# Performance work log

Hardware: AMD Instinct MI355X
Metric: run time of the kernel (lower is better)

The kernel has to match this reference:

```python
import jax, jax.numpy as jnp
import numpy as np

# Module constants (from init_kwargs)
TRUNC = (32, 32, 32)
OUT_SIZE = (32, 32, 32)
HOMOMORPHIC = False


def dct2_ortho_mat(N):
    """Orthonormal DCT-II matrix C of shape [N, N]; y = C @ x along an axis.
    IDCT (DCT-III ortho) is C.T since C is orthogonal."""
    n = jnp.arange(N, dtype=jnp.float32)          # sample index
    k = n[:, None]                                 # frequency index
    C = jnp.cos(jnp.pi * (2.0 * n + 1.0) * k / (2.0 * N))
    scale = jnp.where(k == 0, jnp.sqrt(1.0 / N), jnp.sqrt(2.0 / N))
    return (C * scale).astype(jnp.float32)


def _transform3d(x, Cd, Ch, Cw):
    # Apply separable 1D transforms along D, H, W axes of [B, C, D, H, W].
    x = jnp.einsum('kd,bcdhw->bckhw', Cd, x)
    x = jnp.einsum('kh,bcdhw->bcdkw', Ch, x)
    x = jnp.einsum('kw,bcdhw->bcdhk', Cw, x)
    return x


def setup_inputs() -> dict:
    key = jax.random.key(0)
    x = jax.random.normal(key, (4, 32, 64, 64, 64), dtype=jnp.float32)
    return {"x": x}


def reference(x) -> jnp.ndarray:
    B, C, D, H, W = x.shape
    if HOMOMORPHIC:
        x = jnp.log(x + 1e-6)

    # 3D DCT-II (ortho) along D, H, W
    Cd, Ch, Cw = dct2_ortho_mat(D), dct2_ortho_mat(H), dct2_ortho_mat(W)
    x_dct = _transform3d(x, Cd, Ch, Cw)

    # Crop low frequencies to `truncation`, zero-pad up to `output_size`
    t0, t1, t2 = TRUNC
    o0, o1, o2 = OUT_SIZE
    x_crop = x_dct[:, :, :t0, :t1, :t2]
    x_pad = jnp.pad(x_crop, ((0, 0), (0, 0), (0, o0 - t0), (0, o1 - t1), (0, o2 - t2)))

    # 3D IDCT (DCT-III ortho) = transpose of the ortho DCT-II matrix
    Id, Ih, Iw = dct2_ortho_mat(o0).T, dct2_ortho_mat(o1).T, dct2_ortho_mat(o2).T
    out = _transform3d(x_pad, Id, Ih, Iw)

    if HOMOMORPHIC:
        out = jnp.exp(out)
    return out
```

## Files before the change

kernel.cpp:

```cpp
#include <hip/hip_runtime.h>
#include <math.h>
#include <stdint.h>


#define PI_F 3.14159265358979323846f

typedef __attribute__((ext_vector_type(4))) float f32x4;
typedef __attribute__((ext_vector_type(8))) short bf16x8;

union U16x8 { uint4 q; bf16x8 v; };

__device__ __forceinline__ unsigned short bf16r(float x) {
    union { float f; uint32_t u; } c; c.f = x;
    uint32_t r = (c.u + 0x7FFFu + ((c.u >> 16) & 1u)) >> 16;
    return (unsigned short)r;
}

__device__ __forceinline__ float Aelem(int i, int d) {
    const float s1 = sqrtf(1.0f / 32.0f), s2 = sqrtf(2.0f / 32.0f);
    const float t1 = sqrtf(1.0f / 64.0f), t2 = sqrtf(2.0f / 64.0f);
    float acc = 0.f;
    for (int k = 0; k < 32; ++k) {
        int n1 = ((2 * i + 1) * k) & 127;
        int n2 = ((2 * d + 1) * k) & 255;
        float c1 = cosf((float)n1 * (PI_F / 64.0f));
        float c2 = cosf((float)n2 * (PI_F / 128.0f));
        acc += ((k == 0) ? s1 : s2) * ((k == 0) ? t1 : t2) * c1 * c2;
    }
    return acc;
}

__global__ __launch_bounds__(256) void build_tables(float* __restrict__ At,
                                                    unsigned short* __restrict__ F) {
    int e = blockIdx.x * 256 + threadIdx.x;
    if (e < 2048) {
        int d = e >> 5, i = e & 31;
        At[e] = Aelem(i, d);
    } else if (e < 4096) {
        int f = e - 2048;
        int jj = f & 7, lane = (f >> 3) & 63, tk = f >> 9;
        int tt = tk >> 1, kt = tk & 1;
        int row = tt * 16 + (lane & 15);
        int col = kt * 32 + ((lane >> 4) << 3) + jj;
        F[f] = bf16r(Aelem(row, col));
    }
}

__global__ __launch_bounds__(256) void k_hw(const float* __restrict__ x,
                                            const unsigned short* __restrict__ F,
                                            unsigned short* __restrict__ w1b) {
    __shared__ unsigned short Ut[4][2048];
    __shared__ float Ob[4][32 * 36];

    const int t = threadIdx.x;
    const int wv = t >> 6, ln = t & 63;
    const int lm = ln & 15, lg = ln >> 4;
    const size_t slab = (size_t)blockIdx.x * 4 + wv;

    bf16x8 Ff[2][2];
    {
        const uint4* fp = (const uint4*)F;
        #pragma unroll
        for (int tt = 0; tt < 2; ++tt)
            #pragma unroll
            for (int kt = 0; kt < 2; ++kt) {
                U16x8 u; u.q = fp[(tt * 2 + kt) * 64 + ln];
                Ff[tt][kt] = u.v;
            }
    }

    const float* xs = x + slab * 4096;
    f32x4 accu[4][2];
    #pragma unroll
    for (int mt = 0; mt < 4; ++mt)
        #pragma unroll
        for (int nt = 0; nt < 2; ++nt)
            accu[mt][nt] = (f32x4){0.f, 0.f, 0.f, 0.f};

    #pragma unroll
    for (int mt = 0; mt < 4; ++mt) {
        #pragma unroll
        for (int kt = 0; kt < 2; ++kt) {
            const float4* p = (const float4*)(xs + (mt * 16 + lm) * 64 + kt * 32 + (lg << 3));
            float4 a = p[0], b = p[1];
            bf16x8 xf;
            xf[0] = (short)bf16r(a.x); xf[1] = (short)bf16r(a.y);
            xf[2] = (short)bf16r(a.z); xf[3] = (short)bf16r(a.w);
            xf[4] = (short)bf16r(b.x); xf[5] = (short)bf16r(b.y);
            xf[6] = (short)bf16r(b.z); xf[7] = (short)bf16r(b.w);
            #pragma unroll
            for (int nt = 0; nt < 2; ++nt)
                accu[mt][nt] = __builtin_amdgcn_mfma_f32_16x16x32_bf16(
                    xf, Ff[nt][kt], accu[mt][nt], 0, 0, 0);
        }
    }

    unsigned short* ut = Ut[wv];
    #pragma unroll
    for (int mt = 0; mt < 4; ++mt)
        #pragma unroll
        for (int nt = 0; nt < 2; ++nt) {
            int lo = nt * 16 + lm;
            int h0 = mt * 16 + (lg << 2);
            uint32_t w0 = (uint32_t)bf16r(accu[mt][nt][0]) |
                          ((uint32_t)bf16r(accu[mt][nt][1]) << 16);
            uint32_t w1v = (uint32_t)bf16r(accu[mt][nt][2]) |
                           ((uint32_t)bf16r(accu[mt][nt][3]) << 16);
            uint32_t byte = (uint32_t)(lo * 128 + 2 * h0);
            byte ^= (uint32_t)((lo & 7) << 4);
            *(uint2*)((char*)ut + byte) = make_uint2(w0, w1v);
        }
    __builtin_amdgcn_wave_barrier();

    f32x4 acco[2][2];
    #pragma unroll
    for (int mt = 0; mt < 2; ++mt)
        #pragma unroll
        for (int nt = 0; nt < 2; ++nt)
            acco[mt][nt] = (f32x4){0.f, 0.f, 0.f, 0.f};

    #pragma unroll
    for (int mt = 0; mt < 2; ++mt) {
        #pragma unroll
        for (int kt = 0; kt < 2; ++kt) {
            int lo = mt * 16 + lm;
            uint32_t byte = (uint32_t)(lo * 128 + kt * 64 + (lg << 4));
            byte ^= (uint32_t)((lo & 7) << 4);
            bf16x8 uf = *(const bf16x8*)((const char*)ut + byte);
            #pragma unroll
            for (int nt = 0; nt < 2; ++nt)
                acco[mt][nt] = __builtin_amdgcn_mfma_f32_16x16x32_bf16(
                    uf, Ff[nt][kt], acco[mt][nt], 0, 0, 0);
        }
    }

    float* ob = Ob[wv];
    #pragma unroll
    for (int mt = 0; mt < 2; ++mt)
        #pragma unroll
        for (int nt = 0; nt < 2; ++nt)
            #pragma unroll
            for (int r = 0; r < 4; ++r) {
                int lo = mt * 16 + (lg << 2) + r;
                int j  = nt * 16 + lm;
                ob[j * 36 + lo] = acco[mt][nt][r];
            }
    __builtin_amdgcn_wave_barrier();

    const int row = ln >> 1, half = ln & 1;
    const float4* obv = (const float4*)(ob + row * 36 + half * 16);
    float4 o0 = obv[0], o1 = obv[1], o2 = obv[2], o3 = obv[3];
    uint4 q0, q1;
    q0.x = (uint32_t)bf16r(o0.x) | ((uint32_t)bf16r(o0.y) << 16);
    q0.y = (uint32_t)bf16r(o0.z) | ((uint32_t)bf16r(o0.w) << 16);
    q0.z = (uint32_t)bf16r(o1.x) | ((uint32_t)bf16r(o1.y) << 16);
    q0.w = (uint32_t)bf16r(o1.z) | ((uint32_t)bf16r(o1.w) << 16);
    q1.x = (uint32_t)bf16r(o2.x) | ((uint32_t)bf16r(o2.y) << 16);
    q1.y = (uint32_t)bf16r(o2.z) | ((uint32_t)bf16r(o2.w) << 16);
    q1.z = (uint32_t)bf16r(o3.x) | ((uint32_t)bf16r(o3.y) << 16);
    q1.w = (uint32_t)bf16r(o3.z) | ((uint32_t)bf16r(o3.w) << 16);
    uint4* dst = (uint4*)(w1b + slab * 1024 + row * 32 + half * 16);
    dst[0] = q0;
    dst[1] = q1;
}

__global__ __launch_bounds__(256) void k_d(const unsigned short* __restrict__ w1b,
                                           const float* __restrict__ At,
                                           float* __restrict__ out) {
    const int t = threadIdx.x;
    const int bc = blockIdx.x >> 3;
    const int kh = (blockIdx.x >> 2) & 1;
    const int q  = blockIdx.x & 3;
    const int p  = q * 256 + t;
    const unsigned short* src = w1b + (size_t)bc * 65536 + p;
    float acc[16];
    #pragma unroll
    for (int k = 0; k < 16; ++k) acc[k] = 0.f;
    #pragma unroll 8
    for (int d = 0; d < 64; ++d) {
        uint32_t u = (uint32_t)src[d * 1024];
        float v = __uint_as_float(u << 16);
        const float* arow = At + d * 32 + kh * 16;
        #pragma unroll
        for (int k = 0; k < 16; ++k) acc[k] += arow[k] * v;
    }
    float* dst = out + (size_t)bc * 32768 + (size_t)kh * 16384 + p;
    #pragma unroll
    for (int k = 0; k < 16; ++k) dst[k * 1024] = acc[k];
}

extern "C" void kernel_launch(void* const* d_in, const int* in_sizes, int n_in,
                              void* d_out, int out_size, void* d_ws, size_t ws_size,
                              hipStream_t stream) {
    const float* x = (const float*)d_in[0];
    float* out = (float*)d_out;

    float* At          = (float*)d_ws;
    unsigned short* F  = (unsigned short*)((char*)d_ws + 8192);
    unsigned short* w1b = (unsigned short*)((char*)d_ws + 16384);

    build_tables<<<16, 256, 0, stream>>>(At, F);
    k_hw<<<2048, 256, 0, stream>>>(x, F, w1b);
    k_d<<<1024, 256, 0, stream>>>(w1b, At, out);
}
```

Baseline: 46.67 us.

## Hoist input loads, drop LDS output transpose, widen k_d to two columns per thread

After: 55.03 us. +17.9%, slower.

```diff
diff --git a/kernel.cpp b/kernel.cpp
--- a/kernel.cpp
+++ b/kernel.cpp
@@ -14,6 +14,9 @@
     union { float f; uint32_t u; } c; c.f = x;
     uint32_t r = (c.u + 0x7FFFu + ((c.u >> 16) & 1u)) >> 16;
     return (unsigned short)r;
+}
+__device__ __forceinline__ uint32_t bfpack(float a, float b) {
+    return (uint32_t)bf16r(a) | ((uint32_t)bf16r(b) << 16);
 }
 
 __device__ __forceinline__ float Aelem(int i, int d) {
@@ -46,17 +49,27 @@
     }
 }
 
-__global__ __launch_bounds__(256) void k_hw(const float* __restrict__ x,
-                                            const unsigned short* __restrict__ F,
-                                            unsigned short* __restrict__ w1b) {
+__global__ __launch_bounds__(256, 3) void k_hw(const float* __restrict__ x,
+                                               const unsigned short* __restrict__ F,
+                                               unsigned short* __restrict__ w1b) {
     __shared__ unsigned short Ut[4][2048];
-    __shared__ float Ob[4][32 * 36];
 
     const int t = threadIdx.x;
     const int wv = t >> 6, ln = t & 63;
     const int lm = ln & 15, lg = ln >> 4;
     const size_t slab = (size_t)blockIdx.x * 4 + wv;
 
+    const float* xs = x + slab * 4096;
+    uint4 raw[16];
+    #pragma unroll
+    for (int mt = 0; mt < 4; ++mt)
+        #pragma unroll
+        for (int kt = 0; kt < 2; ++kt) {
+            const uint4* p = (const uint4*)(xs + (mt * 16 + lm) * 64 + kt * 32 + (lg << 3));
+            raw[(mt * 2 + kt) * 2 + 0] = p[0];
+            raw[(mt * 2 + kt) * 2 + 1] = p[1];
+        }
+
     bf16x8 Ff[2][2];
     {
         const uint4* fp = (const uint4*)F;
@@ -69,7 +82,6 @@
             }
     }
 
-    const float* xs = x + slab * 4096;
     f32x4 accu[4][2];
     #pragma unroll
     for (int mt = 0; mt < 4; ++mt)
@@ -81,13 +93,10 @@
     for (int mt = 0; mt < 4; ++mt) {
         #pragma unroll
         for (int kt = 0; kt < 2; ++kt) {
-            const float4* p = (const float4*)(xs + (mt * 16 + lm) * 64 + kt * 32 + (lg << 3));
-            float4 a = p[0], b = p[1];
+            const float* f0 = (const float*)&raw[(mt * 2 + kt) * 2];
             bf16x8 xf;
-            xf[0] = (short)bf16r(a.x); xf[1] = (short)bf16r(a.y);
-            xf[2] = (short)bf16r(a.z); xf[3] = (short)bf16r(a.w);
-            xf[4] = (short)bf16r(b.x); xf[5] = (short)bf16r(b.y);
-            xf[6] = (short)bf16r(b.z); xf[7] = (short)bf16r(b.w);
+            #pragma unroll
+            for (int e = 0; e < 8; ++e) xf[e] = (short)bf16r(f0[e]);
             #pragma unroll
             for (int nt = 0; nt < 2; ++nt)
                 accu[mt][nt] = __builtin_amdgcn_mfma_f32_16x16x32_bf16(
@@ -102,10 +111,8 @@
         for (int nt = 0; nt < 2; ++nt) {
             int lo = nt * 16 + lm;
             int h0 = mt * 16 + (lg << 2);
-            uint32_t w0 = (uint32_t)bf16r(accu[mt][nt][0]) |
-                          ((uint32_t)bf16r(accu[mt][nt][1]) << 16);
-            uint32_t w1v = (uint32_t)bf16r(accu[mt][nt][2]) |
-                           ((uint32_t)bf16r(accu[mt][nt][3]) << 16);
+            uint32_t w0 = bfpack(accu[mt][nt][0], accu[mt][nt][1]);
+            uint32_t w1v = bfpack(accu[mt][nt][2], accu[mt][nt][3]);
             uint32_t byte = (uint32_t)(lo * 128 + 2 * h0);
             byte ^= (uint32_t)((lo & 7) << 4);
             *(uint2*)((char*)ut + byte) = make_uint2(w0, w1v);
@@ -134,59 +141,47 @@
         }
     }
 
-    float* ob = Ob[wv];
     #pragma unroll
     for (int mt = 0; mt < 2; ++mt)
         #pragma unroll
-        for (int nt = 0; nt < 2; ++nt)
-            #pragma unroll
-            for (int r = 0; r < 4; ++r) {
-                int lo = mt * 16 + (lg << 2) + r;
-                int j  = nt * 16 + lm;
-                ob[j * 36 + lo] = acco[mt][nt][r];
-            }
-    __builtin_amdgcn_wave_barrier();
-
-    const int row = ln >> 1, half = ln & 1;
-    const float4* obv = (const float4*)(ob + row * 36 + half * 16);
-    float4 o0 = obv[0], o1 = obv[1], o2 = obv[2], o3 = obv[3];
-    uint4 q0, q1;
-    q0.x = (uint32_t)bf16r(o0.x) | ((uint32_t)bf16r(o0.y) << 16);
-    q0.y = (uint32_t)bf16r(o0.z) | ((uint32_t)bf16r(o0.w) << 16);
-    q0.z = (uint32_t)bf16r(o1.x) | ((uint32_t)bf16r(o1.y) << 16);
-    q0.w = (uint32_t)bf16r(o1.z) | ((uint32_t)bf16r(o1.w) << 16);
-    q1.x = (uint32_t)bf16r(o2.x) | ((uint32_t)bf16r(o2.y) << 16);
-    q1.y = (uint32_t)bf16r(o2.z) | ((uint32_t)bf16r(o2.w) << 16);
-    q1.z = (uint32_t)bf16r(o3.x) | ((uint32_t)bf16r(o3.y) << 16);
-    q1.w = (uint32_t)bf16r(o3.z) | ((uint32_t)bf16r(o3.w) << 16);
-    uint4* dst = (uint4*)(w1b + slab * 1024 + row * 32 + half * 16);
-    dst[0] = q0;
-    dst[1] = q1;
-}
-
-__global__ __launch_bounds__(256) void k_d(const unsigned short* __restrict__ w1b,
-                                           const float* __restrict__ At,
-                                           float* __restrict__ out) {
+        for (int nt = 0; nt < 2; ++nt) {
+            uint32_t u0 = bfpack(acco[mt][nt][0], acco[mt][nt][1]);
+            uint32_t u1 = bfpack(acco[mt][nt][2], acco[mt][nt][3]);
+            int j  = nt * 16 + lm;
+            int l0 = mt * 16 + (lg << 2);
+            *(uint2*)(w1b + slab * 1024 + j * 32 + l0) = make_uint2(u0, u1);
+        }
+}
+
+__global__ __launch_bounds__(256, 4) void k_d(const unsigned short* __restrict__ w1b,
+                                              const float* __restrict__ At,
+                                              float* __restrict__ out) {
     const int t = threadIdx.x;
-    const int bc = blockIdx.x >> 3;
-    const int kh = (blockIdx.x >> 2) & 1;
-    const int q  = blockIdx.x & 3;
-    const int p  = q * 256 + t;
-    const unsigned short* src = w1b + (size_t)bc * 65536 + p;
-    float acc[16];
-    #pragma unroll
-    for (int k = 0; k < 16; ++k) acc[k] = 0.f;
+    const int bc = blockIdx.x >> 2;
+    const int kh = (blockIdx.x >> 1) & 1;
+    const int pq = blockIdx.x & 1;
+    const int p0 = pq * 512 + t * 2;
+    const unsigned short* src = w1b + (size_t)bc * 65536 + p0;
+    float acc0[16], acc1[16];
+    #pragma unroll
+    for (int k = 0; k < 16; ++k) { acc0[k] = 0.f; acc1[k] = 0.f; }
     #pragma unroll 8
     for (int d = 0; d < 64; ++d) {
-        uint32_t u = (uint32_t)src[d * 1024];
-        float v = __uint_as_float(u << 16);
+        uint32_t u = *(const uint32_t*)(src + d * 1024);
+        float v0 = __uint_as_float(u << 16);
+        float v1 = __uint_as_float(u & 0xFFFF0000u);
         const float* arow = At + d * 32 + kh * 16;
         #pragma unroll
-        for (int k = 0; k < 16; ++k) acc[k] += arow[k] * v;
-    }
-    float* dst = out + (size_t)bc * 32768 + (size_t)kh * 16384 + p;
-    #pragma unroll
-    for (int k = 0; k < 16; ++k) dst[k * 1024] = acc[k];
+        for (int k = 0; k < 16; ++k) {
+            float a = arow[k];
+            acc0[k] += a * v0;
+            acc1[k] += a * v1;
+        }
+    }
+    float* dst = out + (size_t)bc * 32768 + (size_t)kh * 16384 + p0;
+    #pragma unroll
+    for (int k = 0; k < 16; ++k)
+        *(float2*)(dst + k * 1024) = make_float2(acc0[k], acc1[k]);
 }
 
 extern "C" void kernel_launch(void* const* d_in, const int* in_sizes, int n_in,
@@ -195,11 +190,11 @@
     const float* x = (const float*)d_in[0];
     float* out = (float*)d_out;
 
-    float* At          = (float*)d_ws;
-    unsigned short* F  = (unsigned short*)((char*)d_ws + 8192);
+    float* At           = (float*)d_ws;
+    unsigned short* F   = (unsigned short*)((char*)d_ws + 8192);
     unsigned short* w1b = (unsigned short*)((char*)d_ws + 16384);
 
     build_tables<<<16, 256, 0, stream>>>(At, F);
     k_hw<<<2048, 256, 0, stream>>>(x, F, w1b);
-    k_d<<<1024, 256, 0, stream>>>(w1b, At, out);
-}
+    k_d<<<512, 256, 0, stream>>>(w1b, At, out);
+}
```

## Process two slabs per wave with all global loads issued upfront

Applied to the files above, without the earlier changes.

Result: slower. 48.28 us (+3.4%).

```diff
diff --git a/kernel.cpp b/kernel.cpp
--- a/kernel.cpp
+++ b/kernel.cpp
@@ -14,6 +14,9 @@
     union { float f; uint32_t u; } c; c.f = x;
     uint32_t r = (c.u + 0x7FFFu + ((c.u >> 16) & 1u)) >> 16;
     return (unsigned short)r;
+}
+__device__ __forceinline__ uint32_t bfpack(float a, float b) {
+    return (uint32_t)bf16r(a) | ((uint32_t)bf16r(b) << 16);
 }
 
 __device__ __forceinline__ float Aelem(int i, int d) {
@@ -46,16 +49,82 @@
     }
 }
 
-__global__ __launch_bounds__(256) void k_hw(const float* __restrict__ x,
-                                            const unsigned short* __restrict__ F,
-                                            unsigned short* __restrict__ w1b) {
+#define PROCESS_SLAB(RAW, SLAB)                                                     \
+    {                                                                               \
+        f32x4 accu[4][2];                                                           \
+        _Pragma("unroll")                                                           \
+        for (int mt = 0; mt < 4; ++mt)                                              \
+            _Pragma("unroll")                                                       \
+            for (int nt = 0; nt < 2; ++nt)                                          \
+                accu[mt][nt] = (f32x4){0.f, 0.f, 0.f, 0.f};                         \
+        _Pragma("unroll")                                                           \
+        for (int mt = 0; mt < 4; ++mt)                                              \
+            _Pragma("unroll")                                                       \
+            for (int kt = 0; kt < 2; ++kt) {                                        \
+                const float* f0 = (const float*)&RAW[(mt * 2 + kt) * 2];            \
+                bf16x8 xf;                                                          \
+                _Pragma("unroll")                                                   \
+                for (int e = 0; e < 8; ++e) xf[e] = (short)bf16r(f0[e]);            \
+                _Pragma("unroll")                                                   \
+                for (int nt = 0; nt < 2; ++nt)                                      \
+                    accu[mt][nt] = __builtin_amdgcn_mfma_f32_16x16x32_bf16(         \
+                        xf, Ff[nt][kt], accu[mt][nt], 0, 0, 0);                     \
+            }                                                                       \
+        _Pragma("unroll")                                                           \
+        for (int mt = 0; mt < 4; ++mt)                                              \
+            _Pragma("unroll")                                                       \
+            for (int nt = 0; nt < 2; ++nt) {                                        \
+                int lo = nt * 16 + lm;                                              \
+                int h0 = mt * 16 + (lg << 2);                                       \
+                uint32_t w0 = bfpack(accu[mt][nt][0], accu[mt][nt][1]);             \
+                uint32_t w1v = bfpack(accu[mt][nt][2], accu[mt][nt][3]);            \
+                uint32_t byte = (uint32_t)(lo * 128 + 2 * h0);                      \
+                byte ^= (uint32_t)((lo & 7) << 4);                                  \
+                *(uint2*)((char*)ut + byte) = make_uint2(w0, w1v);                  \
+            }                                                                       \
+        __builtin_amdgcn_wave_barrier();                                            \
+        f32x4 acco[2][2];                                                           \
+        _Pragma("unroll")                                                           \
+        for (int mt = 0; mt < 2; ++mt)                                              \
+            _Pragma("unroll")                                                       \
+            for (int nt = 0; nt < 2; ++nt)                                          \
+                acco[mt][nt] = (f32x4){0.f, 0.f, 0.f, 0.f};                         \
+        _Pragma("unroll")                                                           \
+        for (int mt = 0; mt < 2; ++mt)                                              \
+            _Pragma("unroll")                                                       \
+            for (int kt = 0; kt < 2; ++kt) {                                        \
+                int lo = mt * 16 + lm;                                              \
+                uint32_t byte = (uint32_t)(lo * 128 + kt * 64 + (lg << 4));         \
+                byte ^= (uint32_t)((lo & 7) << 4);                                  \
+                bf16x8 uf = *(const bf16x8*)((const char*)ut + byte);               \
+                _Pragma("unroll")                                                   \
+                for (int nt = 0; nt < 2; ++nt)                                      \
+                    acco[mt][nt] = __builtin_amdgcn_mfma_f32_16x16x32_bf16(         \
+                        uf, Ff[nt][kt], acco[mt][nt], 0, 0, 0);                     \
+            }                                                                       \
+        _Pragma("unroll")                                                           \
+        for (int mt = 0; mt < 2; ++mt)                                              \
+            _Pragma("unroll")                                                       \
+            for (int nt = 0; nt < 2; ++nt) {                                        \
+                uint32_t u0 = bfpack(acco[mt][nt][0], acco[mt][nt][1]);             \
+                uint32_t u1 = bfpack(acco[mt][nt][2], acco[mt][nt][3]);             \
+                int j  = nt * 16 + lm;                                              \
+                int l0 = mt * 16 + (lg << 2);                                       \
+                *(uint2*)(w1b + (SLAB) * 1024 + j * 32 + l0) = make_uint2(u0, u1);  \
+            }                                                                       \
+        __builtin_amdgcn_wave_barrier();                                            \
+    }
+
+__global__ __launch_bounds__(256, 2) void k_hw(const float* __restrict__ x,
+                                               const unsigned short* __restrict__ F,
+                                               unsigned short* __restrict__ w1b) {
     __shared__ unsigned short Ut[4][2048];
-    __shared__ float Ob[4][32 * 36];
 
     const int t = threadIdx.x;
     const int wv = t >> 6, ln = t & 63;
     const int lm = ln & 15, lg = ln >> 4;
-    const size_t slab = (size_t)blockIdx.x * 4 + wv;
+    const size_t slab0 = (size_t)blockIdx.x * 8 + wv * 2;
+    unsigned short* ut = Ut[wv];
 
     bf16x8 Ff[2][2];
     {
@@ -69,99 +138,28 @@
             }
     }
 
-    const float* xs = x + slab * 4096;
-    f32x4 accu[4][2];
+    const float* xs0 = x + slab0 * 4096;
+    const float* xs1 = xs0 + 4096;
+    uint4 raw0[16], raw1[16];
     #pragma unroll
     for (int mt = 0; mt < 4; ++mt)
         #pragma unroll
-        for (int nt = 0; nt < 2; ++nt)
-            accu[mt][nt] = (f32x4){0.f, 0.f, 0.f, 0.f};
-
-    #pragma unroll
-    for (int mt = 0; mt < 4; ++mt) {
-        #pragma unroll
         for (int kt = 0; kt < 2; ++kt) {
-            const float4* p = (const float4*)(xs + (mt * 16 + lm) * 64 + kt * 32 + (lg << 3));
-            float4 a = p[0], b = p[1];
-            bf16x8 xf;
-            xf[0] = (short)bf16r(a.x); xf[1] = (short)bf16r(a.y);
-            xf[2] = (short)bf16r(a.z); xf[3] = (short)bf16r(a.w);
-            xf[4] = (short)bf16r(b.x); xf[5] = (short)bf16r(b.y);
-            xf[6] = (short)bf16r(b.z); xf[7] = (short)bf16r(b.w);
-            #pragma unroll
-            for (int nt = 0; nt < 2; ++nt)
-                accu[mt][nt] = __builtin_amdgcn_mfma_f32_16x16x32_bf16(
-                    xf, Ff[nt][kt], accu[mt][nt], 0, 0, 0);
+            const uint4* p = (const uint4*)(xs0 + (mt * 16 + lm) * 64 + kt * 32 + (lg << 3));
+            raw0[(mt * 2 + kt) * 2 + 0] = p[0];
+            raw0[(mt * 2 + kt) * 2 + 1] = p[1];
         }
-    }
-
-    unsigned short* ut = Ut[wv];
     #pragma unroll
     for (int mt = 0; mt < 4; ++mt)
         #pragma unroll
-        for (int nt = 0; nt < 2; ++nt) {
-            int lo = nt * 16 + lm;
-            int h0 = mt * 16 + (lg << 2);
-            uint32_t w0 = (uint32_t)bf16r(accu[mt][nt][0]) |
-                          ((uint32_t)bf16r(accu[mt][nt][1]) << 16);
-            uint32_t w1v = (uint32_t)bf16r(accu[mt][nt][2]) |
-                           ((uint32_t)bf16r(accu[mt][nt][3]) << 16);
-            uint32_t byte = (uint32_t)(lo * 128 + 2 * h0);
-            byte ^= (uint32_t)((lo & 7) << 4);
-            *(uint2*)((char*)ut + byte) = make_uint2(w0, w1v);
+        for (int kt = 0; kt < 2; ++kt) {
+            const uint4* p = (const uint4*)(xs1 + (mt * 16 + lm) * 64 + kt * 32 + (lg << 3));
+            raw1[(mt * 2 + kt) * 2 + 0] = p[0];
+            raw1[(mt * 2 + kt) * 2 + 1] = p[1];
         }
-    __builtin_amdgcn_wave_barrier();
-
-    f32x4 acco[2][2];
-    #pragma unroll
-    for (int mt = 0; mt < 2; ++mt)
-        #pragma unroll
-        for (int nt = 0; nt < 2; ++nt)
-            acco[mt][nt] = (f32x4){0.f, 0.f, 0.f, 0.f};
-
-    #pragma unroll
-    for (int mt = 0; mt < 2; ++mt) {
-        #pragma unroll
-        for (int kt = 0; kt < 2; ++kt) {
-            int lo = mt * 16 + lm;
-            uint32_t byte = (uint32_t)(lo * 128 + kt * 64 + (lg << 4));
-            byte ^= (uint32_t)((lo & 7) << 4);
-            bf16x8 uf = *(const bf16x8*)((const char*)ut + byte);
-            #pragma unroll
-            for (int nt = 0; nt < 2; ++nt)
-                acco[mt][nt] = __builtin_amdgcn_mfma_f32_16x16x32_bf16(
-                    uf, Ff[nt][kt], acco[mt][nt], 0, 0, 0);
-        }
-    }
-
-    float* ob = Ob[wv];
-    #pragma unroll
-    for (int mt = 0; mt < 2; ++mt)
-        #pragma unroll
-        for (int nt = 0; nt < 2; ++nt)
-            #pragma unroll
-            for (int r = 0; r < 4; ++r) {
-                int lo = mt * 16 + (lg << 2) + r;
-                int j  = nt * 16 + lm;
-                ob[j * 36 + lo] = acco[mt][nt][r];
-            }
-    __builtin_amdgcn_wave_barrier();
-
-    const int row = ln >> 1, half = ln & 1;
-    const float4* obv = (const float4*)(ob + row * 36 + half * 16);
-    float4 o0 = obv[0], o1 = obv[1], o2 = obv[2], o3 = obv[3];
-    uint4 q0, q1;
-    q0.x = (uint32_t)bf16r(o0.x) | ((uint32_t)bf16r(o0.y) << 16);
-    q0.y = (uint32_t)bf16r(o0.z) | ((uint32_t)bf16r(o0.w) << 16);
-    q0.z = (uint32_t)bf16r(o1.x) | ((uint32_t)bf16r(o1.y) << 16);
-    q0.w = (uint32_t)bf16r(o1.z) | ((uint32_t)bf16r(o1.w) << 16);
-    q1.x = (uint32_t)bf16r(o2.x) | ((uint32_t)bf16r(o2.y) << 16);
-    q1.y = (uint32_t)bf16r(o2.z) | ((uint32_t)bf16r(o2.w) << 16);
-    q1.z = (uint32_t)bf16r(o3.x) | ((uint32_t)bf16r(o3.y) << 16);
-    q1.w = (uint32_t)bf16r(o3.z) | ((uint32_t)bf16r(o3.w) << 16);
-    uint4* dst = (uint4*)(w1b + slab * 1024 + row * 32 + half * 16);
-    dst[0] = q0;
-    dst[1] = q1;
+
+    PROCESS_SLAB(raw0, slab0)
+    PROCESS_SLAB(raw1, (slab0 + 1))
 }
 
 __global__ __launch_bounds__(256) void k_d(const unsigned short* __restrict__ w1b,
@@ -195,11 +193,11 @@
     const float* x = (const float*)d_in[0];
     float* out = (float*)d_out;
 
-    float* At          = (float*)d_ws;
-    unsigned short* F  = (unsigned short*)((char*)d_ws + 8192);
+    float* At           = (float*)d_ws;
+    unsigned short* F   = (unsigned short*)((char*)d_ws + 8192);
     unsigned short* w1b = (unsigned short*)((char*)d_ws + 16384);
 
     build_tables<<<16, 256, 0, stream>>>(At, F);
-    k_hw<<<2048, 256, 0, stream>>>(x, F, w1b);
+    k_hw<<<1024, 256, 0, stream>>>(x, F, w1b);
     k_d<<<1024, 256, 0, stream>>>(w1b, At, out);
 }
```
